# Optimization experiments

Measured on AMD Instinct MI355X. Metric: run time of the kernel, lower is better.

## Reference

```python
import jax, jax.numpy as jnp
import numpy as np

B, S, D, H = 2, 2048, 1024, 16
AD = D // H  # per-head dim = 64


def setup_inputs() -> dict:
    key = jax.random.key(0)
    k1, k2, k3 = jax.random.split(key, 3)
    x = jax.random.normal(k1, (B, S, D), dtype=jnp.float32)
    W_qkv = jax.random.normal(k2, (D, 3 * D), dtype=jnp.float32) * (1.0 / np.sqrt(D))
    b_qkv = jax.random.normal(k3, (3 * D,), dtype=jnp.float32) * 0.01
    return {"x": x, "W_qkv": W_qkv, "b_qkv": b_qkv}


def reference(x, W_qkv, b_qkv):
    b, s, _ = x.shape
    qkv = x @ W_qkv + b_qkv                      # [B,S,3D]
    qkv = qkv.reshape(b, s, H, 3 * AD)           # per-head interleaved qkv
    qkv = jnp.transpose(qkv, (0, 2, 1, 3))       # [B,H,S,3*ad]
    q = qkv[..., :AD]
    k = qkv[..., AD:2 * AD]
    v = qkv[..., 2 * AD:]
    scale = 1.0 / jnp.sqrt(jnp.asarray(AD, dtype=x.dtype))
    att = jnp.einsum("bhqd,bhkd->bhqk", q, k) * scale  # [B,H,S,S]
    att = jax.nn.softmax(att, axis=-1)
    values = jnp.einsum("bhqk,bhkd->bhqd", att, v)     # [B,H,S,ad]
    # Faithful to source: reshape [B,H,S,ad] -> [B,S,ad*H] WITHOUT head transpose
    return values.reshape(b, s, AD * H)
```

## Files before the change

kernel.cpp:

```cpp
#include <hip/hip_runtime.h>
#include <stdint.h>
#include <stddef.h>

#define S_LEN 2048
#define NH 16
#define HD 64
#define DM 1024
#define NQKV 3072
#define MROWS 4096
#define NBH 32

typedef float f32x4 __attribute__((ext_vector_type(4)));
typedef __bf16 bf16x8 __attribute__((ext_vector_type(8)));
typedef __bf16 bf16x4 __attribute__((ext_vector_type(4)));
typedef short short8_t __attribute__((ext_vector_type(8)));

__device__ __forceinline__ unsigned short f2bf(float f) {
  union { float f; unsigned int u; } v; v.f = f;
  unsigned int u = v.u;
  u += 0x7FFFu + ((u >> 16) & 1u);
  return (unsigned short)(u >> 16);
}

__device__ __forceinline__ void async_copy16(const void* g, void* l) {
  __builtin_amdgcn_global_load_lds(
      (const __attribute__((address_space(1))) void*)g,
      (__attribute__((address_space(3))) void*)l, 16, 0, 0);
}

__global__ __launch_bounds__(256) void cast_x_kernel(const float* __restrict__ x,
                                                     unsigned short* __restrict__ xb) {
  size_t i = ((size_t)blockIdx.x * 256 + threadIdx.x) * 8;
  f32x4 a = *(const f32x4*)(x + i);
  f32x4 b = *(const f32x4*)(x + i + 4);
  union { unsigned short u[8]; short8_t v; } o;
  o.u[0] = f2bf(a[0]); o.u[1] = f2bf(a[1]); o.u[2] = f2bf(a[2]); o.u[3] = f2bf(a[3]);
  o.u[4] = f2bf(b[0]); o.u[5] = f2bf(b[1]); o.u[6] = f2bf(b[2]); o.u[7] = f2bf(b[3]);
  *(short8_t*)(xb + i) = o.v;
}

__global__ __launch_bounds__(256) void transpose_w_kernel(const float* __restrict__ W,
                                                          unsigned short* __restrict__ wt) {
  __shared__ float tile[32][33];
  const int n0 = blockIdx.x * 32;
  const int k0 = blockIdx.y * 32;
  const int tx = threadIdx.x;
  const int ty = threadIdx.y;
  #pragma unroll
  for (int i = 0; i < 4; ++i)
    tile[ty + i * 8][tx] = W[(size_t)(k0 + ty + i * 8) * NQKV + n0 + tx];
  __syncthreads();
  #pragma unroll
  for (int i = 0; i < 4; ++i)
    wt[(size_t)(n0 + ty + i * 8) * DM + k0 + tx] = f2bf(tile[tx][ty + i * 8]);
}

__global__ __launch_bounds__(256) void qkv_gemm_kernel(
    const unsigned short* __restrict__ xb, const unsigned short* __restrict__ wt,
    const float* __restrict__ bias,
    unsigned short* __restrict__ Qb, unsigned short* __restrict__ Kb,
    unsigned short* __restrict__ Vt) {
  __shared__ __align__(16) unsigned char Sh[4][128 * 64 * 2];
  const int t = threadIdx.x;
  const int lane = t & 63;
  const int wave = t >> 6;
  const int wm = (wave >> 1) * 64, wn = (wave & 1) * 64;
  const int lr = lane & 15, g = lane >> 4;
  const int m0 = blockIdx.x * 128, n0 = blockIdx.y * 128;

  f32x4 acc[4][4];
  #pragma unroll
  for (int i = 0; i < 4; ++i)
    #pragma unroll
    for (int j = 0; j < 4; ++j) acc[i][j] = f32x4{0.f, 0.f, 0.f, 0.f};

  auto stage = [&](int kt, int buf) __attribute__((always_inline)) {
    const int k0 = kt * 64;
    #pragma unroll
    for (int i = 0; i < 4; ++i) {
      int c = t + i * 256;
      int row = c >> 3;
      int cc = (c & 7) ^ (row & 7);
      async_copy16(xb + (size_t)(m0 + row) * DM + k0 + cc * 8, Sh[buf * 2] + c * 16);
      async_copy16(wt + (size_t)(n0 + row) * DM + k0 + cc * 8, Sh[buf * 2 + 1] + c * 16);
    }
  };

  auto compute = [&](int buf) __attribute__((always_inline)) {
    unsigned char* const As = Sh[buf * 2];
    unsigned char* const Bs = Sh[buf * 2 + 1];
    bf16x8 af[2][4], bfr[2][4];
    #pragma unroll
    for (int kk = 0; kk < 2; ++kk) {
      #pragma unroll
      for (int i = 0; i < 4; ++i) {
        int ra = wm + i * 16 + lr;
        af[kk][i] = *(const bf16x8*)(As + ((ra * 128 + kk * 64 + g * 16) ^ ((ra & 7) << 4)));
        int rb = wn + i * 16 + lr;
        bfr[kk][i] = *(const bf16x8*)(Bs + ((rb * 128 + kk * 64 + g * 16) ^ ((rb & 7) << 4)));
      }
    }
    __builtin_amdgcn_s_setprio(1);
    #pragma unroll
    for (int kk = 0; kk < 2; ++kk)
      #pragma unroll
      for (int mi = 0; mi < 4; ++mi)
        #pragma unroll
        for (int ni = 0; ni < 4; ++ni)
          acc[mi][ni] = __builtin_amdgcn_mfma_f32_16x16x32_bf16(
              af[kk][mi], bfr[kk][ni], acc[mi][ni], 0, 0, 0);
    __builtin_amdgcn_s_setprio(0);
  };

  stage(0, 0);
  __syncthreads();
  for (int kt = 0; kt < DM / 64; kt += 2) {
    stage(kt + 1, 1);
    compute(0);
    __syncthreads();
    if (kt + 2 < DM / 64) stage(kt + 2, 0);
    compute(1);
    __syncthreads();
  }

  const float QSC = 0.18033688011112042f;
  const int nbase = n0 + wn;
  const int h = nbase / 192;
  const int typ = (nbase % 192) >> 6;
  const int b = m0 >> 11;
  const int bh = b * NH + h;

  if (typ == 2) {
    unsigned char* const T = Sh[0] + wave * 8192;
    #pragma unroll
    for (int ni = 0; ni < 4; ++ni) {
      int col = ni * 16 + lr;
      float bv = bias[nbase + col];
      #pragma unroll
      for (int mi = 0; mi < 4; ++mi) {
        bf16x4 w;
        w[0] = (__bf16)(acc[mi][ni][0] + bv);
        w[1] = (__bf16)(acc[mi][ni][1] + bv);
        w[2] = (__bf16)(acc[mi][ni][2] + bv);
        w[3] = (__bf16)(acc[mi][ni][3] + bv);
        int byte = (col * 128 + (mi * 16 + g * 4) * 2) ^ ((col & 7) << 4);
        *(bf16x4*)(T + byte) = w;
      }
    }
    asm volatile("s_waitcnt lgkmcnt(0)" ::: "memory");
    __builtin_amdgcn_sched_barrier(0);
    const int s0 = (m0 & 2047) + wm + (lane & 7) * 8;
    #pragma unroll
    for (int i = 0; i < 8; ++i) {
      int col = i * 8 + (lane >> 3);
      int byte = (col * 128 + (lane & 7) * 16) ^ ((col & 7) << 4);
      bf16x8 v = *(const bf16x8*)(T + byte);
      *(bf16x8*)(Vt + ((size_t)bh * HD + col) * S_LEN + s0) = v;
    }
  } else {
    unsigned short* const dst = (typ == 0) ? Qb : Kb;
    const float sc = (typ == 0) ? QSC : 1.0f;
    #pragma unroll
    for (int ni = 0; ni < 4; ++ni) {
      int d = ni * 16 + lr;
      float bv = bias[nbase + d];
      #pragma unroll
      for (int mi = 0; mi < 4; ++mi) {
        #pragma unroll
        for (int r = 0; r < 4; ++r) {
          int s = (m0 & 2047) + wm + mi * 16 + g * 4 + r;
          dst[((size_t)bh * S_LEN + s) * HD + d] = f2bf((acc[mi][ni][r] + bv) * sc);
        }
      }
    }
  }
}

__global__ __launch_bounds__(512) void attn_kernel(
    const unsigned short* __restrict__ Qb, const unsigned short* __restrict__ Kb,
    const unsigned short* __restrict__ Vt, float* __restrict__ out) {
  __shared__ __align__(16) unsigned char Ks[2][64 * 128];
  __shared__ __align__(16) unsigned char Vs[2][64 * 128];
  __shared__ __align__(16) unsigned char Ps[8][16 * 128];
  const int t = threadIdx.x;
  const int lane = t & 63;
  const int wave = t >> 6;
  const int lr = lane & 15, g = lane >> 4;
  const int bh = blockIdx.y;
  const int q0 = blockIdx.x * 128 + wave * 16;

  const unsigned short* Qbh = Qb + (size_t)bh * S_LEN * HD;
  const unsigned short* Kbh = Kb + (size_t)bh * S_LEN * HD;
  const unsigned short* Vbh = Vt + (size_t)bh * HD * S_LEN;

  bf16x8 qf[2];
  #pragma unroll
  for (int kk = 0; kk < 2; ++kk)
    qf[kk] = *(const bf16x8*)(Qbh + (size_t)(q0 + lr) * HD + kk * 32 + g * 8);

  union { unsigned short u[8]; bf16x8 v; } one_c;
  #pragma unroll
  for (int j = 0; j < 8; ++j) one_c.u[j] = 0x3F80;
  const bf16x8 ones8 = one_c.v;

  int kvOff[4][2];
  #pragma unroll
  for (int i = 0; i < 4; ++i)
    #pragma unroll
    for (int kk = 0; kk < 2; ++kk) {
      int r = i * 16 + lr;
      kvOff[i][kk] = (r * 128 + kk * 64 + g * 16) ^ ((r & 7) << 4);
    }
  unsigned char* const Pw = Ps[wave];
  int pWr[4];
  #pragma unroll
  for (int ni = 0; ni < 4; ++ni)
    pWr[ni] = (lr * 128 + ni * 32 + g * 8) ^ ((lr & 7) << 4);

  const int c0 = t;
  const int row0 = c0 >> 3;
  const int cc0 = (c0 & 7) ^ (row0 & 7);
  const int kGO0 = row0 * HD + cc0 * 8;
  const int vGO0 = row0 * S_LEN + cc0 * 8;

  f32x4 lacc = f32x4{0.f, 0.f, 0.f, 0.f};
  f32x4 oacc[4];
  #pragma unroll
  for (int di = 0; di < 4; ++di) oacc[di] = f32x4{0.f, 0.f, 0.f, 0.f};

  auto stage = [&](int kt, int buf) __attribute__((always_inline)) {
    const unsigned short* kp = Kbh + (size_t)kt * (64 * HD);
    const unsigned short* vp = Vbh + kt * 64;
    async_copy16(kp + kGO0, &Ks[buf][c0 * 16]);
    async_copy16(vp + vGO0, &Vs[buf][c0 * 16]);
  };

  auto compute = [&](int buf) __attribute__((always_inline)) {
    f32x4 sacc[4];
    #pragma unroll
    for (int ni = 0; ni < 4; ++ni) sacc[ni] = f32x4{-8.f, -8.f, -8.f, -8.f};
    __builtin_amdgcn_s_setprio(1);
    #pragma unroll
    for (int ni = 0; ni < 4; ++ni)
      #pragma unroll
      for (int kk = 0; kk < 2; ++kk) {
        bf16x8 kf = *(const bf16x8*)(&Ks[buf][kvOff[ni][kk]]);
        sacc[ni] = __builtin_amdgcn_mfma_f32_16x16x32_bf16(kf, qf[kk], sacc[ni], 0, 0, 0);
      }
    __builtin_amdgcn_s_setprio(0);

    #pragma unroll
    for (int ni = 0; ni < 4; ++ni) {
      bf16x4 w;
      w[0] = (__bf16)exp2f(sacc[ni][0]);
      w[1] = (__bf16)exp2f(sacc[ni][1]);
      w[2] = (__bf16)exp2f(sacc[ni][2]);
      w[3] = (__bf16)exp2f(sacc[ni][3]);
      *(bf16x4*)(Pw + pWr[ni]) = w;
    }

    bf16x8 pf[2];
    #pragma unroll
    for (int kk = 0; kk < 2; ++kk)
      pf[kk] = *(const bf16x8*)(Pw + kvOff[0][kk]);
    __builtin_amdgcn_s_setprio(1);
    #pragma unroll
    for (int di = 0; di < 4; ++di)
      #pragma unroll
      for (int kk = 0; kk < 2; ++kk) {
        bf16x8 vf = *(const bf16x8*)(&Vs[buf][kvOff[di][kk]]);
        oacc[di] = __builtin_amdgcn_mfma_f32_16x16x32_bf16(vf, pf[kk], oacc[di], 0, 0, 0);
      }
    #pragma unroll
    for (int kk = 0; kk < 2; ++kk)
      lacc = __builtin_amdgcn_mfma_f32_16x16x32_bf16(ones8, pf[kk], lacc, 0, 0, 0);
    __builtin_amdgcn_s_setprio(0);
  };

  stage(0, 0);
  __syncthreads();

  for (int kt = 0; kt < S_LEN / 64; kt += 2) {
    stage(kt + 1, 1);
    compute(0);
    __syncthreads();
    if (kt + 2 < S_LEN / 64) stage(kt + 2, 0);
    compute(1);
    __syncthreads();
  }

  float inv = 1.0f / lacc[0];
  float* outp = out + ((size_t)bh * S_LEN + q0 + lr) * HD;
  #pragma unroll
  for (int di = 0; di < 4; ++di) {
    f32x4 o = oacc[di] * inv;
    *(f32x4*)(outp + di * 16 + g * 4) = o;
  }
}

extern "C" void kernel_launch(void* const* d_in, const int* in_sizes, int n_in,
                              void* d_out, int out_size, void* d_ws, size_t ws_size,
                              hipStream_t stream) {
  const float* x    = (const float*)d_in[0];
  const float* W    = (const float*)d_in[1];
  const float* bias = (const float*)d_in[2];
  float* out = (float*)d_out;

  unsigned short* xb = (unsigned short*)d_ws;
  unsigned short* wt = xb + (size_t)MROWS * DM;
  unsigned short* Qb = wt + (size_t)NQKV * DM;
  unsigned short* Kb = Qb + (size_t)NBH * S_LEN * HD;
  unsigned short* Vt = Kb + (size_t)NBH * S_LEN * HD;

  cast_x_kernel<<<(MROWS * DM) / (256 * 8), 256, 0, stream>>>(x, xb);
  transpose_w_kernel<<<dim3(NQKV / 32, DM / 32), dim3(32, 8), 0, stream>>>(W, wt);
  qkv_gemm_kernel<<<dim3(MROWS / 128, NQKV / 128), 256, 0, stream>>>(xb, wt, bias, Qb, Kb, Vt);
  attn_kernel<<<dim3(S_LEN / 128, NBH), 512, 0, stream>>>(Qb, Kb, Vt, out);
}
```

Baseline: 98.08 us.

## Deepen attention K/V prefetch to four LDS buffers with explicit vmcnt waits

```diff
diff --git a/kernel.cpp b/kernel.cpp
--- a/kernel.cpp
+++ b/kernel.cpp
@@ -27,6 +27,12 @@
       (const __attribute__((address_space(1))) void*)g,
       (__attribute__((address_space(3))) void*)l, 16, 0, 0);
 }
+
+#define WAITCNT_BARRIER(N)                                          \
+  asm volatile("s_waitcnt vmcnt(" #N ")" ::: "memory");             \
+  __builtin_amdgcn_sched_barrier(0);                                \
+  __builtin_amdgcn_s_barrier();                                     \
+  __builtin_amdgcn_sched_barrier(0);
 
 __global__ __launch_bounds__(256) void cast_x_kernel(const float* __restrict__ x,
                                                      unsigned short* __restrict__ xb) {
@@ -179,9 +185,7 @@
 __global__ __launch_bounds__(512) void attn_kernel(
     const unsigned short* __restrict__ Qb, const unsigned short* __restrict__ Kb,
     const unsigned short* __restrict__ Vt, float* __restrict__ out) {
-  __shared__ __align__(16) unsigned char Ks[2][64 * 128];
-  __shared__ __align__(16) unsigned char Vs[2][64 * 128];
-  __shared__ __align__(16) unsigned char Ps[8][16 * 128];
+  __shared__ __align__(16) unsigned char smem[81920];
   const int t = threadIdx.x;
   const int lane = t & 63;
   const int wave = t >> 6;
@@ -211,7 +215,7 @@
       int r = i * 16 + lr;
       kvOff[i][kk] = (r * 128 + kk * 64 + g * 16) ^ ((r & 7) << 4);
     }
-  unsigned char* const Pw = Ps[wave];
+  unsigned char* const Pw = smem + 65536 + wave * 2048;
   int pWr[4];
   #pragma unroll
   for (int ni = 0; ni < 4; ++ni)
@@ -231,11 +235,14 @@
   auto stage = [&](int kt, int buf) __attribute__((always_inline)) {
     const unsigned short* kp = Kbh + (size_t)kt * (64 * HD);
     const unsigned short* vp = Vbh + kt * 64;
-    async_copy16(kp + kGO0, &Ks[buf][c0 * 16]);
-    async_copy16(vp + vGO0, &Vs[buf][c0 * 16]);
+    unsigned char* const base = smem + buf * 16384;
+    async_copy16(kp + kGO0, base + c0 * 16);
+    async_copy16(vp + vGO0, base + 8192 + c0 * 16);
   };
 
   auto compute = [&](int buf) __attribute__((always_inline)) {
+    unsigned char* const Ksb = smem + buf * 16384;
+    unsigned char* const Vsb = Ksb + 8192;
     f32x4 sacc[4];
     #pragma unroll
     for (int ni = 0; ni < 4; ++ni) sacc[ni] = f32x4{-8.f, -8.f, -8.f, -8.f};
@@ -244,7 +251,7 @@
     for (int ni = 0; ni < 4; ++ni)
       #pragma unroll
       for (int kk = 0; kk < 2; ++kk) {
-        bf16x8 kf = *(const bf16x8*)(&Ks[buf][kvOff[ni][kk]]);
+        bf16x8 kf = *(const bf16x8*)(Ksb + kvOff[ni][kk]);
         sacc[ni] = __builtin_amdgcn_mfma_f32_16x16x32_bf16(kf, qf[kk], sacc[ni], 0, 0, 0);
       }
     __builtin_amdgcn_s_setprio(0);
@@ -268,7 +275,7 @@
     for (int di = 0; di < 4; ++di)
       #pragma unroll
       for (int kk = 0; kk < 2; ++kk) {
-        bf16x8 vf = *(const bf16x8*)(&Vs[buf][kvOff[di][kk]]);
+        bf16x8 vf = *(const bf16x8*)(Vsb + kvOff[di][kk]);
         oacc[di] = __builtin_amdgcn_mfma_f32_16x16x32_bf16(vf, pf[kk], oacc[di], 0, 0, 0);
       }
     #pragma unroll
@@ -278,16 +285,17 @@
   };
 
   stage(0, 0);
-  __syncthreads();
-
-  for (int kt = 0; kt < S_LEN / 64; kt += 2) {
-    stage(kt + 1, 1);
-    compute(0);
-    __syncthreads();
-    if (kt + 2 < S_LEN / 64) stage(kt + 2, 0);
-    compute(1);
-    __syncthreads();
+  stage(1, 1);
+  for (int kt4 = 0; kt4 < 28; kt4 += 4) {
+    stage(kt4 + 2, 2); WAITCNT_BARRIER(4); compute(0);
+    stage(kt4 + 3, 3); WAITCNT_BARRIER(4); compute(1);
+    stage(kt4 + 4, 0); WAITCNT_BARRIER(4); compute(2);
+    stage(kt4 + 5, 1); WAITCNT_BARRIER(4); compute(3);
   }
+  stage(30, 2); WAITCNT_BARRIER(4); compute(0);
+  stage(31, 3); WAITCNT_BARRIER(4); compute(1);
+  WAITCNT_BARRIER(2); compute(2);
+  WAITCNT_BARRIER(0); compute(3);
 
   float inv = 1.0f / lacc[0];
   float* outp = out + ((size_t)bh * S_LEN + q0 + lr) * HD;
```

Result: no change. 96.24 us (-1.9%).
